# Kernel optimization log

Measured on AMD Instinct MI355X. Metric: run time of the kernel, lower is better.

The kernel has to match this reference:

```python
import jax, jax.numpy as jnp
import numpy as np

B, D, LC, LQ = 64, 128, 1000, 100


def setup_inputs() -> dict:
    key = jax.random.key(0)
    kc, kq, kw = jax.random.split(key, 3)
    C = jax.random.normal(kc, (B, D, LC), dtype=jnp.float32)
    Q = jax.random.normal(kq, (B, D, LQ), dtype=jnp.float32)
    # xavier_normal over fan_in=1 rows x fan_out=3D cols per [1, 3D] slice
    std = float(np.sqrt(2.0 / (1 + 3 * D)))
    W = jax.random.normal(kw, (B * LC, 1, 3 * D), dtype=jnp.float32) * std
    return {"C": C, "Q": Q, "W": W}


def reference(C, Q, W):
    # C: [B, D, Lc], Q: [B, D, Lq], W: [B*Lc, 1, 3D]
    Ct = jnp.transpose(C, (0, 2, 1))  # [B, Lc, D]
    Qt = jnp.transpose(Q, (0, 2, 1))  # [B, Lq, D]
    Wr = W.reshape(B, LC, 3 * D)
    w1, w2, w3 = Wr[:, :, :D], Wr[:, :, D:2 * D], Wr[:, :, 2 * D:]
    # Trilinear similarity decomposed into three terms (concat order: [Qi, C, Q*C])
    S = (
        jnp.einsum("bid,bjd->bij", w1, Qt)
        + jnp.sum(w2 * Ct, axis=-1, keepdims=True)
        + jnp.einsum("bid,bjd->bij", w3 * Ct, Qt)
    )  # [B, Lc, Lq]
    S1 = jax.nn.softmax(S, axis=2)  # over query positions
    S2 = jax.nn.softmax(S, axis=1)  # over context positions
    A = jnp.einsum("bij,bjd->bid", S1, Qt)  # context-to-query [B, Lc, D]
    Bm = jnp.einsum("bik,bkd->bid", jnp.einsum("bij,bkj->bik", S1, S2), Ct)
    out = jnp.concatenate([Ct, A, Ct * A, Ct * Bm], axis=2)  # [B, Lc, 4D]
    return jnp.transpose(out, (0, 2, 1))  # [B, 4D, Lc]
```

## Files before the change

kernel.cpp:

```cpp
#include <hip/hip_runtime.h>
#include <cstddef>

#define B_  64
#define D_  128
#define LC_ 1000
#define LQ_ 100
#define SP  104
#define JP  128

__global__ __launch_bounds__(256) void k_transpose(const float* __restrict__ C,
                                                   float* __restrict__ Ct){
  __shared__ float t[32][33];
  int b  = blockIdx.z;
  int i0 = blockIdx.x * 32;
  int d0 = blockIdx.y * 32;
  int tx = threadIdx.x, ty = threadIdx.y;
  const float* Cb  = C  + (size_t)b * D_ * LC_;
  float*       Ctb = Ct + (size_t)b * LC_ * D_;
#pragma unroll
  for(int k=0;k<4;k++){
    int d = d0 + ty + 8*k;
    int i = i0 + tx;
    t[ty+8*k][tx] = (i < LC_) ? Cb[(size_t)d*LC_ + i] : 0.f;
  }
  __syncthreads();
#pragma unroll
  for(int k=0;k<4;k++){
    int i = i0 + ty + 8*k;
    int d = d0 + tx;
    if(i < LC_) Ctb[(size_t)i*D_ + d] = t[tx][ty+8*k];
  }
}

__global__ __launch_bounds__(256) void k_transposeQ(const float* __restrict__ Q,
                                                    float* __restrict__ Qt){
  __shared__ float t[32][33];
  int b  = blockIdx.z;
  int j0 = blockIdx.x * 32;
  int d0 = blockIdx.y * 32;
  int tx = threadIdx.x, ty = threadIdx.y;
  const float* Qb  = Q  + (size_t)b * D_ * LQ_;
  float*       Qtb = Qt + (size_t)b * LQ_ * D_;
#pragma unroll
  for(int k=0;k<4;k++){
    int d = d0 + ty + 8*k;
    int j = j0 + tx;
    t[ty+8*k][tx] = (j < LQ_) ? Qb[(size_t)d*LQ_ + j] : 0.f;
  }
  __syncthreads();
#pragma unroll
  for(int k=0;k<4;k++){
    int j = j0 + ty + 8*k;
    int d = d0 + tx;
    if(j < LQ_) Qtb[(size_t)j*D_ + d] = t[tx][ty+8*k];
  }
}

__global__ __launch_bounds__(256) void k_S(const float* __restrict__ Q,
                                           const float* __restrict__ W,
                                           const float* __restrict__ Ct,
                                           float* __restrict__ S){
  __shared__ float Qs[32][132];
  __shared__ float Vs[64][33];
  __shared__ float t2s[64];
  int b   = blockIdx.y;
  int i0  = blockIdx.x * 64;
  int tid = threadIdx.x;
  const float* Wb  = W  + (size_t)b * LC_ * 384;
  const float* Ctb = Ct + (size_t)b * LC_ * D_;
  const float* Qb  = Q  + (size_t)b * D_ * LQ_;

  {
    int g = tid >> 5, l = tid & 31;
    for(int rep=0; rep<8; rep++){
      int il = rep*8 + g;
      int i  = i0 + il;
      float s = 0.f;
      if(i < LC_){
        const float* wrow  = Wb  + (size_t)i*384 + 128;
        const float* ctrow = Ctb + (size_t)i*D_;
#pragma unroll
        for(int k=0;k<4;k++){ int d = l + 32*k; s += wrow[d]*ctrow[d]; }
      }
#pragma unroll
      for(int m=16;m>0;m>>=1) s += __shfl_xor(s, m, 64);
      if(l==0) t2s[il] = s;
    }
  }

  int jt = tid & 15;
  int ti = tid >> 4;
  float acc[4][8] = {};

  for(int c=0;c<4;c++){
    int dc0 = c*32;
    __syncthreads();
    for(int idx=tid; idx<32*128; idx+=256){
      int dc = idx >> 7, j = idx & 127;
      Qs[dc][j] = (j < LQ_) ? Qb[(size_t)(dc0+dc)*LQ_ + j] : 0.f;
    }
    for(int idx=tid; idx<64*32; idx+=256){
      int il = idx >> 5, dc = idx & 31;
      int i = i0 + il;
      float v = 0.f;
      if(i < LC_){
        const float* wrow = Wb + (size_t)i*384;
        float ct = Ctb[(size_t)i*D_ + dc0+dc];
        v = wrow[dc0+dc] + wrow[256+dc0+dc]*ct;
      }
      Vs[il][dc] = v;
    }
    __syncthreads();
#pragma unroll 4
    for(int dc=0; dc<32; dc++){
      float v[4];
#pragma unroll
      for(int ii=0; ii<4; ii++) v[ii] = Vs[ti*4+ii][dc];
      float4 q0 = *(const float4*)&Qs[dc][jt*8];
      float4 q1 = *(const float4*)&Qs[dc][jt*8+4];
      float q[8] = {q0.x,q0.y,q0.z,q0.w,q1.x,q1.y,q1.z,q1.w};
#pragma unroll
      for(int ii=0; ii<4; ii++)
#pragma unroll
        for(int jj=0; jj<8; jj++) acc[ii][jj] += v[ii]*q[jj];
    }
  }
  float* Sb = S + (size_t)b * LC_ * SP;
#pragma unroll
  for(int ii=0; ii<4; ii++){
    int il = ti*4+ii;
    int i  = i0 + il;
    if(i < LC_){
      float t2v = t2s[il];
      float4 o0, o1;
      o0.x=acc[ii][0]+t2v; o0.y=acc[ii][1]+t2v; o0.z=acc[ii][2]+t2v; o0.w=acc[ii][3]+t2v;
      o1.x=acc[ii][4]+t2v; o1.y=acc[ii][5]+t2v; o1.z=acc[ii][6]+t2v; o1.w=acc[ii][7]+t2v;
      if(jt*8   < SP) *(float4*)&Sb[(size_t)i*SP + jt*8    ] = o0;
      if(jt*8+4 < SP) *(float4*)&Sb[(size_t)i*SP + jt*8 + 4] = o1;
    }
  }
}

#define NIC 8
__global__ __launch_bounds__(256) void k_colstats1(const float* __restrict__ S,
                                                   float* __restrict__ pm,
                                                   float* __restrict__ ps){
  __shared__ float lm[8][128], lsum[8][128];
  int b = blockIdx.x, ic = blockIdx.y;
  int tid = threadIdx.x;
  int jt = tid & 31, h = tid >> 5;
  int j0 = jt*4;
  int ni = min(16, 125 - h*16);
  const float* Sb = S + (size_t)b * LC_ * SP;
  float m[4] = {-1e30f,-1e30f,-1e30f,-1e30f}, s[4] = {0.f,0.f,0.f,0.f};
  if(jt < 26){
    for(int r=0;r<ni;r++){
      int i = ic*125 + h*16 + r;
      float4 x = *(const float4*)&Sb[(size_t)i*SP + j0];
      float xv[4] = {x.x,x.y,x.z,x.w};
#pragma unroll
      for(int k=0;k<4;k++){
        if(xv[k] > m[k]){ s[k] = s[k]*__expf(m[k]-xv[k]) + 1.f; m[k] = xv[k]; }
        else              s[k] += __expf(xv[k]-m[k]);
      }
    }
  }
#pragma unroll
  for(int k=0;k<4;k++){
    int j = j0+k;
    if(j < 128){ lm[h][j] = m[k]; lsum[h][j] = s[k]; }
  }
  __syncthreads();
  if(tid < 128){
    float mm = -1e30f, ss = 0.f;
#pragma unroll
    for(int hh=0; hh<8; hh++){
      float m2 = lm[hh][tid], s2 = lsum[hh][tid];
      if(m2 > mm){ ss = ss*__expf(mm-m2) + s2; mm = m2; }
      else         ss += s2*__expf(m2-mm);
    }
    pm[((size_t)b*NIC + ic)*128 + tid] = mm;
    ps[((size_t)b*NIC + ic)*128 + tid] = ss;
  }
}

__global__ __launch_bounds__(128) void k_colstats2(const float* __restrict__ pm,
                                                   const float* __restrict__ ps,
                                                   float* __restrict__ cm,
                                                   float* __restrict__ cs){
  int b = blockIdx.x, j = threadIdx.x;
  float mm = -1e30f, ss = 0.f;
#pragma unroll
  for(int ic=0; ic<NIC; ic++){
    float m2 = pm[((size_t)b*NIC + ic)*128 + j];
    float s2 = ps[((size_t)b*NIC + ic)*128 + j];
    if(m2 > mm){ ss = ss*__expf(mm-m2) + s2; mm = m2; }
    else         ss += s2*__expf(m2-mm);
  }
  cm[b*JP + j] = mm;
  cs[b*JP + j] = (ss == 0.f) ? 1.f : ss;
}

#define MJQ 25
__global__ __launch_bounds__(1024) void k_Mj(const float* __restrict__ S,
                                             const float* __restrict__ Ct,
                                             const float* __restrict__ cm_,
                                             const float* __restrict__ cs_,
                                             float* __restrict__ M){
  __shared__ float Es[4][16][32];
  __shared__ float Cs[4][16][132];
  __shared__ float Macc[25][132];
  __shared__ float cml[32], icsl[32];
  int b  = blockIdx.x;
  int jq = blockIdx.y;
  int j0 = jq * MJQ;
  int tid = threadIdx.x;
  int grp = tid >> 8;
  int t   = tid & 255;
  if(tid < 32){
    int j = j0 + tid;
    cml[tid]  = (tid < MJQ && j < LQ_) ? cm_[b*JP + j] : 0.f;
    icsl[tid] = (tid < MJQ && j < LQ_) ? 1.f/cs_[b*JP + j] : 0.f;
  }
  __syncthreads();
  int dt = t & 31;
  int jt = t >> 5;
  float acc[4][4] = {};
  const float* Sb  = S  + (size_t)b * LC_ * SP + j0;
  const float* Ctb = Ct + (size_t)b * LC_ * D_;
  int ibase = grp * 250;

  for(int i0=0; i0<250; i0+=16){
    int rem = min(16, 250 - i0);
    __syncthreads();
    for(int idx=t; idx<16*32; idx+=256){
      int ii = idx >> 5, jl = idx & 31;
      float e = 0.f;
      if(ii < rem && jl < MJQ)
        e = __expf(Sb[(size_t)(ibase+i0+ii)*SP + jl] - cml[jl]);
      Es[grp][ii][jl] = e;
    }
    for(int idx=t; idx<16*32; idx+=256){
      int ii = idx >> 5, f = idx & 31;
      float4 v = make_float4(0.f,0.f,0.f,0.f);
      if(ii < rem) v = *(const float4*)&Ctb[(size_t)(ibase+i0+ii)*D_ + f*4];
      *(float4*)&Cs[grp][ii][f*4] = v;
    }
    __syncthreads();
#pragma unroll
    for(int ii=0; ii<16; ii++){
      float4 e4 = *(const float4*)&Es[grp][ii][jt*4];
      float4 c4 = *(const float4*)&Cs[grp][ii][dt*4];
      float e[4] = {e4.x,e4.y,e4.z,e4.w};
      float c[4] = {c4.x,c4.y,c4.z,c4.w};
#pragma unroll
      for(int jj=0; jj<4; jj++)
#pragma unroll
        for(int dd=0; dd<4; dd++) acc[jj][dd] += e[jj]*c[dd];
    }
  }

  for(int g=0; g<4; g++){
    if(grp == g){
#pragma unroll
      for(int jj=0; jj<4; jj++){
        int jl = jt*4 + jj;
        if(jl < MJQ){
#pragma unroll
          for(int dd=0; dd<4; dd++){
            if(g == 0) Macc[jl][dt*4+dd]  = acc[jj][dd];
            else       Macc[jl][dt*4+dd] += acc[jj][dd];
          }
        }
      }
    }
    __syncthreads();
  }
  if(grp == 0){
    float* Mb = M + (size_t)b * JP * D_;
#pragma unroll
    for(int jj=0; jj<4; jj++){
      int jl = jt*4 + jj;
      if(jl < MJQ && (j0+jl) < LQ_){
        float ics = icsl[jl];
        float4 o;
        o.x = Macc[jl][dt*4+0]*ics; o.y = Macc[jl][dt*4+1]*ics;
        o.z = Macc[jl][dt*4+2]*ics; o.w = Macc[jl][dt*4+3]*ics;
        *(float4*)&Mb[(size_t)(j0+jl)*D_ + dt*4] = o;
      }
    }
  }
}

__global__ __launch_bounds__(256) void k_final(const float* __restrict__ S,
                                               const float* __restrict__ Qt,
                                               const float* __restrict__ M,
                                               const float* __restrict__ C,
                                               float* __restrict__ out){
  __shared__ float lds[10880];
  float* S1s = lds;
  float* Qc  = lds + 6656;
  float* Mc  = lds + 8768;
  float* At  = lds;
  int b   = blockIdx.y;
  int i0  = blockIdx.x * 64;
  int tid = threadIdx.x;
  const float* Sb  = S  + (size_t)b * LC_ * SP;
  const float* Qtb = Qt + (size_t)b * LQ_ * D_;
  const float* Mb  = M  + (size_t)b * JP * D_;

  for(int idx=tid; idx<64*26; idx+=256){
    int il = idx / 26, f = idx % 26;
    int i = i0 + il;
    float4 v = make_float4(0.f,0.f,0.f,0.f);
    if(i < LC_ && f < 25) v = *(const float4*)&Sb[(size_t)i*SP + f*4];
    *(float4*)&S1s[il*104 + f*4] = v;
  }
  __syncthreads();

  {
    int w = tid >> 6, l = tid & 63;
    for(int r=0; r<16; r++){
      int il = w*16 + r;
      float x0 = (2*l   < LQ_) ? S1s[il*104 + 2*l  ] : -1e30f;
      float x1 = (2*l+1 < LQ_) ? S1s[il*104 + 2*l+1] : -1e30f;
      float m = fmaxf(x0,x1);
#pragma unroll
      for(int mm=32;mm>0;mm>>=1) m = fmaxf(m, __shfl_xor(m, mm, 64));
      float e0 = (2*l   < LQ_) ? __expf(x0-m) : 0.f;
      float e1 = (2*l+1 < LQ_) ? __expf(x1-m) : 0.f;
      float s = e0+e1;
#pragma unroll
      for(int mm=32;mm>0;mm>>=1) s += __shfl_xor(s, mm, 64);
      float inv = 1.f/s;
      if(2*l   < LQ_) S1s[il*104 + 2*l  ] = e0*inv;
      if(2*l+1 < LQ_) S1s[il*104 + 2*l+1] = e1*inv;
    }
  }

  int dt = tid & 31;
  int it = tid >> 5;
  float A[8][4] = {}, Bm[8][4] = {};
  for(int j0=0; j0<LQ_; j0+=16){
    int nj = min(16, LQ_-j0);
    __syncthreads();
    for(int idx=tid; idx<nj*32; idx+=256){
      int jj = idx >> 5, f = idx & 31;
      *(float4*)&Qc[jj*132 + f*4] = *(const float4*)&Qtb[(size_t)(j0+jj)*D_ + f*4];
      *(float4*)&Mc[jj*132 + f*4] = *(const float4*)&Mb [(size_t)(j0+jj)*D_ + f*4];
    }
    __syncthreads();
    for(int jj4=0; jj4<nj; jj4+=4){
      float4 sv[8], qv[4], mv[4];
#pragma unroll
      for(int ii=0; ii<8; ii++) sv[ii] = *(const float4*)&S1s[(it*8+ii)*104 + j0+jj4];
#pragma unroll
      for(int jj=0; jj<4; jj++){
        qv[jj] = *(const float4*)&Qc[(jj4+jj)*132 + dt*4];
        mv[jj] = *(const float4*)&Mc[(jj4+jj)*132 + dt*4];
      }
#pragma unroll
      for(int ii=0; ii<8; ii++){
        float sf[4] = {sv[ii].x, sv[ii].y, sv[ii].z, sv[ii].w};
#pragma unroll
        for(int jj=0; jj<4; jj++){
          A[ii][0]  += sf[jj]*qv[jj].x; A[ii][1]  += sf[jj]*qv[jj].y;
          A[ii][2]  += sf[jj]*qv[jj].z; A[ii][3]  += sf[jj]*qv[jj].w;
          Bm[ii][0] += sf[jj]*mv[jj].x; Bm[ii][1] += sf[jj]*mv[jj].y;
          Bm[ii][2] += sf[jj]*mv[jj].z; Bm[ii][3] += sf[jj]*mv[jj].w;
        }
      }
    }
  }

  const float* Cb = C + (size_t)b * D_ * LC_;
  float* ob = out + (size_t)b * 512 * LC_;
  int il2 = tid & 63, dg = tid >> 6;
  int i = i0 + il2;

  __syncthreads();
#pragma unroll
  for(int ii=0; ii<8; ii++)
#pragma unroll
    for(int dd=0; dd<4; dd++) At[(it*8+ii)*133 + dt*4+dd] = A[ii][dd];
  __syncthreads();
  if(i < LC_){
    for(int dd2=0; dd2<32; dd2++){
      int d = dg*32 + dd2;
      float a = At[il2*133 + d];
      float c = Cb[(size_t)d*LC_ + i];
      ob[(size_t)d*LC_ + i]       = c;
      ob[(size_t)(128+d)*LC_ + i] = a;
      ob[(size_t)(256+d)*LC_ + i] = c*a;
    }
  }
  __syncthreads();
#pragma unroll
  for(int ii=0; ii<8; ii++)
#pragma unroll
    for(int dd=0; dd<4; dd++) At[(it*8+ii)*133 + dt*4+dd] = Bm[ii][dd];
  __syncthreads();
  if(i < LC_){
    for(int dd2=0; dd2<32; dd2++){
      int d = dg*32 + dd2;
      float bm = At[il2*133 + d];
      float c  = Cb[(size_t)d*LC_ + i];
      ob[(size_t)(384+d)*LC_ + i] = c*bm;
    }
  }
}

extern "C" void kernel_launch(void* const* d_in, const int* in_sizes, int n_in,
                              void* d_out, int out_size, void* d_ws, size_t ws_size,
                              hipStream_t stream){
  const float* C = (const float*)d_in[0];
  const float* Q = (const float*)d_in[1];
  const float* W = (const float*)d_in[2];
  float* out = (float*)d_out;
  float* ws  = (float*)d_ws;
  float* S  = ws;
  float* Ct = ws + 6656000;
  float* M  = ws + 14848000;
  float* Qt = ws + 15896576;
  float* pm = ws + 16715776;
  float* ps = ws + 16781312;
  float* cm = ws + 16846848;
  float* cs = ws + 16855040;

  k_transpose <<<dim3(32,4,64), dim3(32,8), 0, stream>>>(C, Ct);
  k_transposeQ<<<dim3(4,4,64),  dim3(32,8), 0, stream>>>(Q, Qt);
  k_S         <<<dim3(16,64),   256, 0, stream>>>(Q, W, Ct, S);
  k_colstats1 <<<dim3(64,NIC),  256, 0, stream>>>(S, pm, ps);
  k_colstats2 <<<64,            128, 0, stream>>>(pm, ps, cm, cs);
  k_Mj        <<<dim3(64,4),    1024, 0, stream>>>(S, Ct, cm, cs, M);
  k_final     <<<dim3(16,64),   256, 0, stream>>>(S, Qt, M, C, out);
}
```

Measured before the change: 421.1 us.

## Vectorize final-kernel output stores, prefetch Q/M chunks, transpose Vs tile

In k_S the V tile in LDS is stored transposed, so each thread reads its four rows with one float4 load instead of four scalar reads. In k_final the Qt/M chunks are prefetched into registers one chunk ahead and written to LDS after the previous chunk's compute. This replaces the two barriers per chunk around a global load with a software-pipelined load. The epilogue is remapped so each thread handles four consecutive context positions and uses float4 global loads of C and float4 stores of out. The cost is more strided, possibly bank-conflicting LDS reads of At, and extra registers for the prefetch.

After: 444.4 us. 5.5% more time.

```diff
diff --git a/kernel.cpp b/kernel.cpp
--- a/kernel.cpp
+++ b/kernel.cpp
@@ -61,7 +61,7 @@
                                            const float* __restrict__ Ct,
                                            float* __restrict__ S){
   __shared__ float Qs[32][132];
-  __shared__ float Vs[64][33];
+  __shared__ float Vs[32][68];
   __shared__ float t2s[64];
   int b   = blockIdx.y;
   int i0  = blockIdx.x * 64;
@@ -108,14 +108,13 @@
         float ct = Ctb[(size_t)i*D_ + dc0+dc];
         v = wrow[dc0+dc] + wrow[256+dc0+dc]*ct;
       }
-      Vs[il][dc] = v;
+      Vs[dc][il] = v;
     }
     __syncthreads();
 #pragma unroll 4
     for(int dc=0; dc<32; dc++){
-      float v[4];
-#pragma unroll
-      for(int ii=0; ii<4; ii++) v[ii] = Vs[ti*4+ii][dc];
+      float4 vv = *(const float4*)&Vs[dc][ti*4];
+      float v[4] = {vv.x, vv.y, vv.z, vv.w};
       float4 q0 = *(const float4*)&Qs[dc][jt*8];
       float4 q1 = *(const float4*)&Qs[dc][jt*8+4];
       float q[8] = {q0.x,q0.y,q0.z,q0.w,q1.x,q1.y,q1.z,q1.w};
@@ -309,6 +308,32 @@
   const float* Qtb = Qt + (size_t)b * LQ_ * D_;
   const float* Mb  = M  + (size_t)b * JP * D_;
 
+  float4 pq[2], pmr[2];
+  auto pfload = [&](int j0c){
+    int nj = min(16, LQ_-j0c);
+#pragma unroll
+    for(int k=0;k<2;k++){
+      int idx = tid + k*256;
+      int jj = idx >> 5, f = idx & 31;
+      if(jj < nj){
+        pq[k]  = *(const float4*)&Qtb[(size_t)(j0c+jj)*D_ + f*4];
+        pmr[k] = *(const float4*)&Mb [(size_t)(j0c+jj)*D_ + f*4];
+      }
+    }
+  };
+  auto pfstore = [&](int j0c){
+    int nj = min(16, LQ_-j0c);
+#pragma unroll
+    for(int k=0;k<2;k++){
+      int idx = tid + k*256;
+      int jj = idx >> 5, f = idx & 31;
+      if(jj < nj){
+        *(float4*)&Qc[jj*132 + f*4] = pq[k];
+        *(float4*)&Mc[jj*132 + f*4] = pmr[k];
+      }
+    }
+  };
+
   for(int idx=tid; idx<64*26; idx+=256){
     int il = idx / 26, f = idx % 26;
     int i = i0 + il;
@@ -316,6 +341,7 @@
     if(i < LC_ && f < 25) v = *(const float4*)&Sb[(size_t)i*SP + f*4];
     *(float4*)&S1s[il*104 + f*4] = v;
   }
+  pfload(0);
   __syncthreads();
 
   {
@@ -337,19 +363,15 @@
       if(2*l+1 < LQ_) S1s[il*104 + 2*l+1] = e1*inv;
     }
   }
+  pfstore(0);
+  pfload(16);
+  __syncthreads();
 
   int dt = tid & 31;
   int it = tid >> 5;
   float A[8][4] = {}, Bm[8][4] = {};
   for(int j0=0; j0<LQ_; j0+=16){
     int nj = min(16, LQ_-j0);
-    __syncthreads();
-    for(int idx=tid; idx<nj*32; idx+=256){
-      int jj = idx >> 5, f = idx & 31;
-      *(float4*)&Qc[jj*132 + f*4] = *(const float4*)&Qtb[(size_t)(j0+jj)*D_ + f*4];
-      *(float4*)&Mc[jj*132 + f*4] = *(const float4*)&Mb [(size_t)(j0+jj)*D_ + f*4];
-    }
-    __syncthreads();
     for(int jj4=0; jj4<nj; jj4+=4){
       float4 sv[8], qv[4], mv[4];
 #pragma unroll
@@ -371,27 +393,37 @@
         }
       }
     }
+    __syncthreads();
+    if(j0+16 < LQ_){
+      pfstore(j0+16);
+      if(j0+32 < LQ_) pfload(j0+32);
+      __syncthreads();
+    }
   }
 
   const float* Cb = C + (size_t)b * D_ * LC_;
   float* ob = out + (size_t)b * 512 * LC_;
-  int il2 = tid & 63, dg = tid >> 6;
-  int i = i0 + il2;
-
-  __syncthreads();
+  int iq = tid & 15, dbase = tid >> 4;
+  int i  = i0 + iq*4;
+  bool iok = (i + 3) < LC_;
+
 #pragma unroll
   for(int ii=0; ii<8; ii++)
 #pragma unroll
     for(int dd=0; dd<4; dd++) At[(it*8+ii)*133 + dt*4+dd] = A[ii][dd];
   __syncthreads();
-  if(i < LC_){
-    for(int dd2=0; dd2<32; dd2++){
-      int d = dg*32 + dd2;
-      float a = At[il2*133 + d];
-      float c = Cb[(size_t)d*LC_ + i];
-      ob[(size_t)d*LC_ + i]       = c;
-      ob[(size_t)(128+d)*LC_ + i] = a;
-      ob[(size_t)(256+d)*LC_ + i] = c*a;
+  if(iok){
+#pragma unroll
+    for(int m=0; m<8; m++){
+      int d = dbase + 16*m;
+      float4 a;
+      a.x = At[(iq*4+0)*133 + d]; a.y = At[(iq*4+1)*133 + d];
+      a.z = At[(iq*4+2)*133 + d]; a.w = At[(iq*4+3)*133 + d];
+      float4 c = *(const float4*)&Cb[(size_t)d*LC_ + i];
+      float4 ca; ca.x=c.x*a.x; ca.y=c.y*a.y; ca.z=c.z*a.z; ca.w=c.w*a.w;
+      *(float4*)&ob[(size_t)d*LC_ + i]        = c;
+      *(float4*)&ob[(size_t)(128+d)*LC_ + i]  = a;
+      *(float4*)&ob[(size_t)(256+d)*LC_ + i]  = ca;
     }
   }
   __syncthreads();
@@ -400,12 +432,16 @@
 #pragma unroll
     for(int dd=0; dd<4; dd++) At[(it*8+ii)*133 + dt*4+dd] = Bm[ii][dd];
   __syncthreads();
-  if(i < LC_){
-    for(int dd2=0; dd2<32; dd2++){
-      int d = dg*32 + dd2;
-      float bm = At[il2*133 + d];
-      float c  = Cb[(size_t)d*LC_ + i];
-      ob[(size_t)(384+d)*LC_ + i] = c*bm;
+  if(iok){
+#pragma unroll
+    for(int m=0; m<8; m++){
+      int d = dbase + 16*m;
+      float4 bm;
+      bm.x = At[(iq*4+0)*133 + d]; bm.y = At[(iq*4+1)*133 + d];
+      bm.z = At[(iq*4+2)*133 + d]; bm.w = At[(iq*4+3)*133 + d];
+      float4 c = *(const float4*)&Cb[(size_t)d*LC_ + i];
+      float4 cb; cb.x=c.x*bm.x; cb.y=c.y*bm.y; cb.z=c.z*bm.z; cb.w=c.w*bm.w;
+      *(float4*)&ob[(size_t)(384+d)*LC_ + i]  = cb;
     }
   }
 }
```
